# Optimization experiments

Hardware: AMD Instinct MI355X
Metric: run time of the kernel (lower is better)

Reference implementation:

```python
import jax, jax.numpy as jnp
import numpy as np

DIM = 512
DIM_HEAD = 64
HEADS = 8
DIM_INNER = DIM_HEAD * HEADS
EPS = float(jnp.finfo(jnp.float32).eps)  # torch nn.RMSNorm default eps


def setup_inputs() -> dict:
    key = jax.random.key(0)
    k1, k2, k3, k4 = jax.random.split(key, 4)
    tokens = jax.random.normal(k1, (2, 4096, DIM), dtype=jnp.float32)
    norm_weight = jnp.ones((DIM,), dtype=jnp.float32)
    s = 1.0 / np.sqrt(DIM)
    w_qkv = jax.random.normal(k2, (DIM, 3 * DIM_INNER), dtype=jnp.float32) * s
    w_out = jax.random.normal(k3, (DIM_INNER, DIM), dtype=jnp.float32) * (1.0 / np.sqrt(DIM_INNER))
    return {"tokens": tokens, "norm_weight": norm_weight, "w_qkv": w_qkv, "w_out": w_out}


def reference(tokens, norm_weight, w_qkv, w_out):
    b, n, d = tokens.shape
    scale = DIM_HEAD ** -0.5
    # RMSNorm
    ms = jnp.mean(jnp.square(tokens), axis=-1, keepdims=True)
    x = tokens * jax.lax.rsqrt(ms + EPS) * norm_weight
    # QKV projection, split heads: b n (qkv h d) -> qkv b h n d
    qkv = x @ w_qkv                                   # [b, n, 3*h*dh]
    qkv = qkv.reshape(b, n, 3, HEADS, DIM_HEAD)
    q, k, v = jnp.moveaxis(qkv, 2, 0)                 # each [b, n, h, dh]
    q = jnp.swapaxes(q, 1, 2)                         # [b, h, n, dh]
    k = jnp.swapaxes(k, 1, 2)
    v = jnp.swapaxes(v, 1, 2)
    # naive attention (note: original applies no scale in forward, self.scale unused)
    sim = jnp.einsum('bhid,bhjd->bhij', q, k)
    attn = jax.nn.softmax(sim, axis=-1)
    out = jnp.einsum('bhij,bhjd->bhid', attn, v)
    out = jnp.swapaxes(out, 1, 2).reshape(b, n, DIM_INNER)
    return out @ w_out
```

## Files before the change

kernel.cpp:

```cpp
#include <hip/hip_runtime.h>
#include <stdint.h>
#include <stddef.h>

typedef _Float16 half_t;
typedef __attribute__((ext_vector_type(2))) __fp16 fp16v2;
typedef __attribute__((ext_vector_type(4))) _Float16 f16x4;
typedef __attribute__((ext_vector_type(8))) _Float16 f16x8;
typedef __attribute__((ext_vector_type(4))) float f32x4;

#define EPSF 1.1920928955078125e-07f
#define LOG2E 1.4426950408889634f

#define AS1 __attribute__((address_space(1)))
#define AS3 __attribute__((address_space(3)))

#define WS_XN   0u
#define WS_WQT  4194304u
#define WS_WOT  4980736u
#define WS_Q    5242880u
#define WS_K    9437184u
#define WS_VT   13631488u
#define WS_AO   17825792u
#define WS_NEED_BYTES 44040192u

__device__ __forceinline__ void gload16(const void* g, void* l) {
  __builtin_amdgcn_global_load_lds((const AS1 void*)g, (AS3 void*)l, 16, 0, 0);
}

__device__ __forceinline__ float fast_exp2(float x) {
#if __has_builtin(__builtin_amdgcn_exp2f)
  return __builtin_amdgcn_exp2f(x);
#else
  return exp2f(x);
#endif
}

__global__ __launch_bounds__(256) void k_rmsnorm(const float* __restrict__ t,
                                                 const float* __restrict__ w,
                                                 half_t* __restrict__ xn) {
  int row = blockIdx.x * 4 + (threadIdx.x >> 6);
  int ln = threadIdx.x & 63;
  const float* src = t + (size_t)row * 512 + ln * 8;
  float4 a = *(const float4*)src;
  float4 b = *(const float4*)(src + 4);
  float ss = a.x * a.x + a.y * a.y + a.z * a.z + a.w * a.w
           + b.x * b.x + b.y * b.y + b.z * b.z + b.w * b.w;
#pragma unroll
  for (int m = 32; m >= 1; m >>= 1) ss += __shfl_xor(ss, m);
  float r = rsqrtf(ss * (1.0f / 512.0f) + EPSF);
  const float* wp = w + ln * 8;
  float4 w0 = *(const float4*)wp;
  float4 w1 = *(const float4*)(wp + 4);
  f16x8 o;
  o[0] = (_Float16)(a.x * r * w0.x);
  o[1] = (_Float16)(a.y * r * w0.y);
  o[2] = (_Float16)(a.z * r * w0.z);
  o[3] = (_Float16)(a.w * r * w0.w);
  o[4] = (_Float16)(b.x * r * w1.x);
  o[5] = (_Float16)(b.y * r * w1.y);
  o[6] = (_Float16)(b.z * r * w1.z);
  o[7] = (_Float16)(b.w * r * w1.w);
  *(f16x8*)(xn + (size_t)row * 512 + ln * 8) = o;
}

__global__ void k_transpose_cast(const float* __restrict__ src, half_t* __restrict__ dst,
                                 int K, int N) {
  int idx = blockIdx.x * 256 + threadIdx.x;
  if (idx >= K * N) return;
  int n = idx / K, k = idx - n * K;
  dst[idx] = (_Float16)src[(size_t)k * N + n];
}

__device__ __forceinline__ void gemm_core(const half_t* __restrict__ A,
                                          const half_t* __restrict__ Bt,
                                          int m0, int n0, int Ksz,
                                          half_t* Al, half_t* Bl,
                                          f32x4 acc[4][4]) {
  int wv = threadIdx.x >> 6, ln = threadIdx.x & 63;
  int wm = (wv >> 1) << 6, wn = (wv & 1) << 6;
  for (int kt = 0; kt < Ksz; kt += 64) {
#pragma unroll
    for (int i = 0; i < 4; ++i) {
      int seg = wv * 4 + i;
      int r = seg * 8 + (ln >> 3);
      int cb = ((ln & 7) * 16) ^ ((r & 7) << 4);
      gload16((const char*)(A + (size_t)(m0 + r) * Ksz + kt) + cb, (char*)Al + seg * 1024);
      gload16((const char*)(Bt + (size_t)(n0 + r) * Ksz + kt) + cb, (char*)Bl + seg * 1024);
    }
    __syncthreads();
#pragma unroll
    for (int kc = 0; kc < 2; ++kc) {
      f16x8 af[4], bf[4];
#pragma unroll
      for (int mt = 0; mt < 4; ++mt) {
        int rr = wm + mt * 16 + (ln & 15);
        af[mt] = *(const f16x8*)((const char*)Al + rr * 128 +
                                 ((kc * 64 + (ln >> 4) * 16) ^ ((rr & 7) << 4)));
      }
#pragma unroll
      for (int nt = 0; nt < 4; ++nt) {
        int rr = wn + nt * 16 + (ln & 15);
        bf[nt] = *(const f16x8*)((const char*)Bl + rr * 128 +
                                 ((kc * 64 + (ln >> 4) * 16) ^ ((rr & 7) << 4)));
      }
#pragma unroll
      for (int mt = 0; mt < 4; ++mt)
#pragma unroll
        for (int nt = 0; nt < 4; ++nt)
          acc[mt][nt] = __builtin_amdgcn_mfma_f32_16x16x32_f16(af[mt], bf[nt], acc[mt][nt], 0, 0, 0);
    }
    __syncthreads();
  }
}

__global__ __launch_bounds__(256, 2) void k_gemm_qkv(const half_t* __restrict__ A,
                                                     const half_t* __restrict__ Bt,
                                                     half_t* __restrict__ q,
                                                     half_t* __restrict__ kk,
                                                     half_t* __restrict__ vt) {
  __shared__ __align__(16) half_t Al[128 * 64];
  __shared__ __align__(16) half_t Bl[128 * 64];
  f32x4 acc[4][4];
  f32x4 z = {0.f, 0.f, 0.f, 0.f};
#pragma unroll
  for (int i = 0; i < 4; ++i)
#pragma unroll
    for (int j = 0; j < 4; ++j) acc[i][j] = z;
  int m0 = blockIdx.x * 128, n0 = blockIdx.y * 128;
  gemm_core(A, Bt, m0, n0, 512, Al, Bl, acc);
  int wv = threadIdx.x >> 6, ln = threadIdx.x & 63;
  int wm = (wv >> 1) << 6, wn = (wv & 1) << 6;
#pragma unroll
  for (int mt = 0; mt < 4; ++mt) {
#pragma unroll
    for (int nt = 0; nt < 4; ++nt) {
      int gn = n0 + wn + nt * 16 + (ln & 15);
      int qkv_i = gn >> 9;
      int h = (gn >> 6) & 7;
      int d = gn & 63;
#pragma unroll
      for (int j = 0; j < 4; ++j) {
        int gm = m0 + wm + mt * 16 + (ln >> 4) * 4 + j;
        int head = ((gm >> 12) << 3) | h;
        int n = gm & 4095;
        float av = acc[mt][nt][j];
        if (qkv_i == 0)      q [((size_t)head * 4096 + n) * 64 + d] = (_Float16)(av * LOG2E);
        else if (qkv_i == 1) kk[((size_t)head * 4096 + n) * 64 + d] = (_Float16)av;
        else                 vt[((size_t)head * 64 + d) * 4096 + n] = (_Float16)av;
      }
    }
  }
}

__global__ __launch_bounds__(256, 2) void k_gemm_out(const half_t* __restrict__ A,
                                                     const half_t* __restrict__ Bt,
                                                     float* __restrict__ out) {
  __shared__ __align__(16) half_t Al[128 * 64];
  __shared__ __align__(16) half_t Bl[128 * 64];
  f32x4 acc[4][4];
  f32x4 z = {0.f, 0.f, 0.f, 0.f};
#pragma unroll
  for (int i = 0; i < 4; ++i)
#pragma unroll
    for (int j = 0; j < 4; ++j) acc[i][j] = z;
  int m0 = blockIdx.x * 128, n0 = blockIdx.y * 128;
  gemm_core(A, Bt, m0, n0, 512, Al, Bl, acc);
  int wv = threadIdx.x >> 6, ln = threadIdx.x & 63;
  int wm = (wv >> 1) << 6, wn = (wv & 1) << 6;
#pragma unroll
  for (int mt = 0; mt < 4; ++mt)
#pragma unroll
    for (int nt = 0; nt < 4; ++nt) {
      int gn = n0 + wn + nt * 16 + (ln & 15);
#pragma unroll
      for (int j = 0; j < 4; ++j) {
        int gm = m0 + wm + mt * 16 + (ln >> 4) * 4 + j;
        out[(size_t)gm * 512 + gn] = acc[mt][nt][j];
      }
    }
}

__global__ __launch_bounds__(256, 2) void k_attn(const half_t* __restrict__ q,
                                                 const half_t* __restrict__ kg,
                                                 const half_t* __restrict__ vt,
                                                 half_t* __restrict__ ao) {
  __shared__ __align__(16) char lds[32768];
  const int wv = threadIdx.x >> 6, ln = threadIdx.x & 63;
  const int bid = blockIdx.x;
  const int lin = (bid & 7) * 64 + (bid >> 3);
  const int head = lin >> 5;
  const int qt = lin & 31;
  const int q0 = qt * 128 + wv * 32;
  const char* qh = (const char*)(q  + (size_t)head * 4096 * 64);
  const char* kh = (const char*)(kg + (size_t)head * 4096 * 64);
  const char* vh = (const char*)(vt + (size_t)head * 64 * 4096);

  f16x8 qf[2][2];
#pragma unroll
  for (int mt = 0; mt < 2; ++mt)
#pragma unroll
    for (int kc = 0; kc < 2; ++kc) {
      int r = q0 + mt * 16 + (ln & 15);
      qf[mt][kc] = *(const f16x8*)(qh + (size_t)r * 128 + kc * 64 + (ln >> 4) * 16);
    }

  const char* ks[2]; const char* vs[2]; int lo[2];
#pragma unroll
  for (int i = 0; i < 2; ++i) {
    int seg = wv * 2 + i;
    int r = seg * 8 + (ln >> 3);
    int cb = ((ln & 7) * 16) ^ ((r & 7) << 4);
    ks[i] = kh + (size_t)r * 128 + cb;
    vs[i] = vh + (size_t)r * 8192 + cb;
    lo[i] = seg * 1024;
  }

  float mrun[2] = {-1e30f, -1e30f};
  float lsum[2] = {0.f, 0.f};
  f32x4 oacc[2][4];
  const f32x4 z = {0.f, 0.f, 0.f, 0.f};
#pragma unroll
  for (int mt = 0; mt < 2; ++mt)
#pragma unroll
    for (int dt = 0; dt < 4; ++dt) oacc[mt][dt] = z;

  {
    char* base = lds;
    gload16(ks[0], base + lo[0]); gload16(ks[1], base + lo[1]);
    gload16(vs[0], base + 8192 + lo[0]); gload16(vs[1], base + 8192 + lo[1]);
    ks[0] += 8192; ks[1] += 8192; vs[0] += 128; vs[1] += 128;
  }
  __syncthreads();

  int cur = 0;
#pragma unroll 1
  for (int t = 0; t < 64; ++t) {
    if (t < 63) {
      char* base = lds + (cur ^ 1) * 16384;
      gload16(ks[0], base + lo[0]); gload16(ks[1], base + lo[1]);
      gload16(vs[0], base + 8192 + lo[0]); gload16(vs[1], base + 8192 + lo[1]);
      ks[0] += 8192; ks[1] += 8192; vs[0] += 128; vs[1] += 128;
    }
    const char* Kb = lds + cur * 16384;
    const char* Vb = Kb + 8192;

    f32x4 s[2][4];
#pragma unroll
    for (int mt = 0; mt < 2; ++mt)
#pragma unroll
      for (int kt = 0; kt < 4; ++kt) s[mt][kt] = z;
    __builtin_amdgcn_s_setprio(1);
#pragma unroll
    for (int kc = 0; kc < 2; ++kc) {
      f16x8 kf[4];
#pragma unroll
      for (int kt = 0; kt < 4; ++kt) {
        int rr = kt * 16 + (ln & 15);
        kf[kt] = *(const f16x8*)(Kb + rr * 128 + ((kc * 64 + (ln >> 4) * 16) ^ ((rr & 7) << 4)));
      }
#pragma unroll
      for (int mt = 0; mt < 2; ++mt)
#pragma unroll
        for (int kt = 0; kt < 4; ++kt)
          s[mt][kt] = __builtin_amdgcn_mfma_f32_16x16x32_f16(kf[kt], qf[mt][kc], s[mt][kt], 0, 0, 0);
    }
    __builtin_amdgcn_s_setprio(0);

    f16x8 pf[2][2];
#pragma unroll
    for (int mt = 0; mt < 2; ++mt) {
      float a0 = fmaxf(fmaxf(s[mt][0][0], s[mt][0][1]), fmaxf(s[mt][0][2], s[mt][0][3]));
      float a1 = fmaxf(fmaxf(s[mt][1][0], s[mt][1][1]), fmaxf(s[mt][1][2], s[mt][1][3]));
      float a2 = fmaxf(fmaxf(s[mt][2][0], s[mt][2][1]), fmaxf(s[mt][2][2], s[mt][2][3]));
      float a3 = fmaxf(fmaxf(s[mt][3][0], s[mt][3][1]), fmaxf(s[mt][3][2], s[mt][3][3]));
      float tm = fmaxf(fmaxf(a0, a1), fmaxf(a2, a3));
      tm = fmaxf(tm, __shfl_xor(tm, 16));
      tm = fmaxf(tm, __shfl_xor(tm, 32));
      if (__any(tm > mrun[mt] + 11.0f)) {
        float mnew = fmaxf(mrun[mt], tm);
        float sc = fast_exp2(mrun[mt] - mnew);
        mrun[mt] = mnew;
        lsum[mt] *= sc;
#pragma unroll
        for (int dt = 0; dt < 4; ++dt) {
          oacc[mt][dt][0] *= sc; oacc[mt][dt][1] *= sc;
          oacc[mt][dt][2] *= sc; oacc[mt][dt][3] *= sc;
        }
      }
      float p[4][4];
#pragma unroll
      for (int kt = 0; kt < 4; ++kt)
#pragma unroll
        for (int r = 0; r < 4; ++r) p[kt][r] = fast_exp2(s[mt][kt][r] - mrun[mt]);
      float ps = 0.f;
#pragma unroll
      for (int kt = 0; kt < 4; ++kt)
        ps += (p[kt][0] + p[kt][1]) + (p[kt][2] + p[kt][3]);
      lsum[mt] += ps;
#pragma unroll
      for (int kc = 0; kc < 2; ++kc) {
        union { f16x8 v; fp16v2 h[4]; } u;
        u.h[0] = __builtin_amdgcn_cvt_pkrtz(p[2 * kc][0], p[2 * kc][1]);
        u.h[1] = __builtin_amdgcn_cvt_pkrtz(p[2 * kc][2], p[2 * kc][3]);
        u.h[2] = __builtin_amdgcn_cvt_pkrtz(p[2 * kc + 1][0], p[2 * kc + 1][1]);
        u.h[3] = __builtin_amdgcn_cvt_pkrtz(p[2 * kc + 1][2], p[2 * kc + 1][3]);
        pf[mt][kc] = u.v;
      }
    }

    __builtin_amdgcn_s_setprio(1);
#pragma unroll
    for (int kc = 0; kc < 2; ++kc)
#pragma unroll
      for (int dt = 0; dt < 4; ++dt) {
        int rr = dt * 16 + (ln & 15);
        int sw = (rr & 7) << 4;
        f16x4 vlo = *(const f16x4*)(Vb + rr * 128 + ((kc * 64 + (ln >> 4) * 8) ^ sw));
        f16x4 vhi = *(const f16x4*)(Vb + rr * 128 + ((kc * 64 + 32 + (ln >> 4) * 8) ^ sw));
        f16x8 vf = __builtin_shufflevector(vlo, vhi, 0, 1, 2, 3, 4, 5, 6, 7);
#pragma unroll
        for (int mt = 0; mt < 2; ++mt)
          oacc[mt][dt] = __builtin_amdgcn_mfma_f32_16x16x32_f16(vf, pf[mt][kc], oacc[mt][dt], 0, 0, 0);
      }
    __builtin_amdgcn_s_setprio(0);

    __syncthreads();
    cur ^= 1;
  }

  const int b = head >> 3, h = head & 7;
#pragma unroll
  for (int mt = 0; mt < 2; ++mt) {
    float l = lsum[mt];
    l += __shfl_xor(l, 16);
    l += __shfl_xor(l, 32);
    float inv = 1.0f / l;
    int n = q0 + mt * 16 + (ln & 15);
    half_t* dst = ao + ((size_t)(b * 4096 + n)) * 512 + h * 64 + (ln >> 4) * 4;
#pragma unroll
    for (int dt = 0; dt < 4; ++dt) {
      f16x4 o4;
      o4[0] = (_Float16)(oacc[mt][dt][0] * inv);
      o4[1] = (_Float16)(oacc[mt][dt][1] * inv);
      o4[2] = (_Float16)(oacc[mt][dt][2] * inv);
      o4[3] = (_Float16)(oacc[mt][dt][3] * inv);
      *(f16x4*)(dst + dt * 16) = o4;
    }
  }
}

extern "C" void kernel_launch(void* const* d_in, const int* in_sizes, int n_in,
                              void* d_out, int out_size, void* d_ws, size_t ws_size,
                              hipStream_t stream) {
  if (ws_size < WS_NEED_BYTES) return;
  const float* tokens = (const float*)d_in[0];
  const float* nw     = (const float*)d_in[1];
  const float* wqkv   = (const float*)d_in[2];
  const float* wout   = (const float*)d_in[3];
  float* out = (float*)d_out;
  half_t* ws = (half_t*)d_ws;
  half_t* xn  = ws + WS_XN;
  half_t* wqt = ws + WS_WQT;
  half_t* wot = ws + WS_WOT;
  half_t* qb  = ws + WS_Q;
  half_t* kb  = ws + WS_K;
  half_t* vtb = ws + WS_VT;
  half_t* aob = ws + WS_AO;

  k_rmsnorm<<<2048, 256, 0, stream>>>(tokens, nw, xn);
  k_transpose_cast<<<(1536 * 512 + 255) / 256, 256, 0, stream>>>(wqkv, wqt, 512, 1536);
  k_transpose_cast<<<(512 * 512 + 255) / 256, 256, 0, stream>>>(wqkv ? wout : wout, wot, 512, 512);
  k_gemm_qkv<<<dim3(64, 12), 256, 0, stream>>>(xn, wqt, qb, kb, vtb);
  k_attn<<<512, 256, 0, stream>>>(qb, kb, vtb, aob);
  k_gemm_out<<<dim3(64, 4), 256, 0, stream>>>(aob, wot, out);
}
```

Measured before the change: 152.9 us.

## Load K tiles straight into registers and compute row sums with MFMA

The attention kernel stops staging K through LDS. Each wave now reads its K fragments directly from global memory into double-buffered registers, one tile ahead, so LDS holds only V and shrinks to 16 KB. The softmax row-sum is accumulated with an extra MFMA against a ones vector, which removes the scalar sums and cross-lane shuffles at the end. V fragment reads are also moved ahead of the softmax math. The cost is that all four waves fetch the same K tile from global/L2, plus higher register pressure and extra tail prefetches past the last tile.

```diff
diff --git a/kernel.cpp b/kernel.cpp
--- a/kernel.cpp
+++ b/kernel.cpp
@@ -184,7 +184,7 @@
                                                  const half_t* __restrict__ kg,
                                                  const half_t* __restrict__ vt,
                                                  half_t* __restrict__ ao) {
-  __shared__ __align__(16) char lds[32768];
+  __shared__ __align__(16) char lds[16384];
   const int wv = threadIdx.x >> 6, ln = threadIdx.x & 63;
   const int bid = blockIdx.x;
   const int lin = (bid & 7) * 64 + (bid >> 3);
@@ -204,137 +204,148 @@
       qf[mt][kc] = *(const f16x8*)(qh + (size_t)r * 128 + kc * 64 + (ln >> 4) * 16);
     }
 
-  const char* ks[2]; const char* vs[2]; int lo[2];
+  const char* kbl = kh + (size_t)(ln & 15) * 128 + (ln >> 4) * 16;
+
+  const char* vs[2]; int lo[2];
 #pragma unroll
   for (int i = 0; i < 2; ++i) {
     int seg = wv * 2 + i;
     int r = seg * 8 + (ln >> 3);
     int cb = ((ln & 7) * 16) ^ ((r & 7) << 4);
-    ks[i] = kh + (size_t)r * 128 + cb;
     vs[i] = vh + (size_t)r * 8192 + cb;
     lo[i] = seg * 1024;
   }
 
   float mrun[2] = {-1e30f, -1e30f};
-  float lsum[2] = {0.f, 0.f};
   f32x4 oacc[2][4];
+  f32x4 lacc[2];
   const f32x4 z = {0.f, 0.f, 0.f, 0.f};
 #pragma unroll
-  for (int mt = 0; mt < 2; ++mt)
+  for (int mt = 0; mt < 2; ++mt) {
+    lacc[mt] = z;
 #pragma unroll
     for (int dt = 0; dt < 4; ++dt) oacc[mt][dt] = z;
-
-  {
-    char* base = lds;
-    gload16(ks[0], base + lo[0]); gload16(ks[1], base + lo[1]);
-    gload16(vs[0], base + 8192 + lo[0]); gload16(vs[1], base + 8192 + lo[1]);
-    ks[0] += 8192; ks[1] += 8192; vs[0] += 128; vs[1] += 128;
-  }
+  }
+  f16x8 ones;
+#pragma unroll
+  for (int e = 0; e < 8; ++e) ones[e] = (_Float16)1.0f;
+
+  f16x8 kA[4][2], kB[4][2];
+
+#define KLOAD(DST, TT) do {                                        \
+    const char* _kb = kbl + (size_t)(TT) * 8192;                   \
+    DST[0][0] = *(const f16x8*)(_kb);                              \
+    DST[0][1] = *(const f16x8*)(_kb + 64);                         \
+    DST[1][0] = *(const f16x8*)(_kb + 2048);                       \
+    DST[1][1] = *(const f16x8*)(_kb + 2112);                       \
+    DST[2][0] = *(const f16x8*)(_kb + 4096);                       \
+    DST[2][1] = *(const f16x8*)(_kb + 4160);                       \
+    DST[3][0] = *(const f16x8*)(_kb + 6144);                       \
+    DST[3][1] = *(const f16x8*)(_kb + 6208);                       \
+  } while (0)
+
+  KLOAD(kA, 0);
+  gload16(vs[0], lds + lo[0]); gload16(vs[1], lds + lo[1]);
+  vs[0] += 128; vs[1] += 128;
   __syncthreads();
 
-  int cur = 0;
+#define TILE_PHASE(KCUR, KNXT, T) {                                            \
+       \
+    KLOAD(KNXT, (T) + 1);                                                      \
+    { char* _base = lds + (((T) + 1) & 1) * 8192;                              \
+      gload16(vs[0], _base + lo[0]); gload16(vs[1], _base + lo[1]);            \
+      vs[0] += 128; vs[1] += 128; }                                            \
+    const char* Vb = lds + ((T) & 1) * 8192;                                   \
+                                                            \
+    f32x4 s[2][4];                                                             \
+    _Pragma("unroll") for (int mt = 0; mt < 2; ++mt)                           \
+      _Pragma("unroll") for (int kt = 0; kt < 4; ++kt) s[mt][kt] = z;          \
+    __builtin_amdgcn_s_setprio(1);                                             \
+    _Pragma("unroll") for (int kc = 0; kc < 2; ++kc)                           \
+      _Pragma("unroll") for (int mt = 0; mt < 2; ++mt)                         \
+        _Pragma("unroll") for (int kt = 0; kt < 4; ++kt)                       \
+          s[mt][kt] = __builtin_amdgcn_mfma_f32_16x16x32_f16(                  \
+              KCUR[kt][kc], qf[mt][kc], s[mt][kt], 0, 0, 0);                   \
+    __builtin_amdgcn_s_setprio(0);                                             \
+                      \
+    f16x8 vf0[4], vf1[4];                                                      \
+    _Pragma("unroll") for (int dt = 0; dt < 4; ++dt) {                         \
+      int rr = dt * 16 + (ln & 15);                                            \
+      int sw = (rr & 7) << 4;                                                  \
+      f16x4 a_ = *(const f16x4*)(Vb + rr * 128 + (((ln >> 4) * 8) ^ sw));      \
+      f16x4 b_ = *(const f16x4*)(Vb + rr * 128 + ((32 + (ln >> 4) * 8) ^ sw)); \
+      vf0[dt] = __builtin_shufflevector(a_, b_, 0, 1, 2, 3, 4, 5, 6, 7);       \
+      f16x4 c_ = *(const f16x4*)(Vb + rr * 128 + ((64 + (ln >> 4) * 8) ^ sw)); \
+      f16x4 d_ = *(const f16x4*)(Vb + rr * 128 + ((96 + (ln >> 4) * 8) ^ sw)); \
+      vf1[dt] = __builtin_shufflevector(c_, d_, 0, 1, 2, 3, 4, 5, 6, 7);       \
+    }                                                                          \
+                      \
+    f16x8 pf[2][2];                                                            \
+    _Pragma("unroll") for (int mt = 0; mt < 2; ++mt) {                         \
+      float a0 = fmaxf(fmaxf(s[mt][0][0], s[mt][0][1]),                        \
+                       fmaxf(s[mt][0][2], s[mt][0][3]));                       \
+      float a1 = fmaxf(fmaxf(s[mt][1][0], s[mt][1][1]),                        \
+                       fmaxf(s[mt][1][2], s[mt][1][3]));                       \
+      float a2 = fmaxf(fmaxf(s[mt][2][0], s[mt][2][1]),                        \
+                       fmaxf(s[mt][2][2], s[mt][2][3]));                       \
+      float a3 = fmaxf(fmaxf(s[mt][3][0], s[mt][3][1]),                        \
+                       fmaxf(s[mt][3][2], s[mt][3][3]));                       \
+      float tm = fmaxf(fmaxf(a0, a1), fmaxf(a2, a3));                          \
+      tm = fmaxf(tm, __shfl_xor(tm, 16));                                      \
+      tm = fmaxf(tm, __shfl_xor(tm, 32));                                      \
+      if (__any(tm > mrun[mt] + 11.0f)) {                                      \
+        float mnew = fmaxf(mrun[mt], tm);                                      \
+        float sc = fast_exp2(mrun[mt] - mnew);                                 \
+        mrun[mt] = mnew;                                                       \
+        lacc[mt][0] *= sc;                                                     \
+        _Pragma("unroll") for (int dt = 0; dt < 4; ++dt) {                     \
+          oacc[mt][dt][0] *= sc; oacc[mt][dt][1] *= sc;                        \
+          oacc[mt][dt][2] *= sc; oacc[mt][dt][3] *= sc;                        \
+        }                                                                      \
+      }                                                                        \
+      float p[4][4];                                                           \
+      _Pragma("unroll") for (int kt = 0; kt < 4; ++kt)                         \
+        _Pragma("unroll") for (int r = 0; r < 4; ++r)                          \
+          p[kt][r] = fast_exp2(s[mt][kt][r] - mrun[mt]);                       \
+      _Pragma("unroll") for (int kc = 0; kc < 2; ++kc) {                       \
+        union { f16x8 v; fp16v2 h[4]; } u;                                     \
+        u.h[0] = __builtin_amdgcn_cvt_pkrtz(p[2 * kc][0], p[2 * kc][1]);       \
+        u.h[1] = __builtin_amdgcn_cvt_pkrtz(p[2 * kc][2], p[2 * kc][3]);       \
+        u.h[2] = __builtin_amdgcn_cvt_pkrtz(p[2 * kc + 1][0], p[2 * kc + 1][1]); \
+        u.h[3] = __builtin_amdgcn_cvt_pkrtz(p[2 * kc + 1][2], p[2 * kc + 1][3]); \
+        pf[mt][kc] = u.v;                                                      \
+      }                                                                        \
+    }                                                                          \
+     \
+    __builtin_amdgcn_s_setprio(1);                                             \
+    _Pragma("unroll") for (int dt = 0; dt < 4; ++dt)                           \
+      _Pragma("unroll") for (int mt = 0; mt < 2; ++mt)                         \
+        oacc[mt][dt] = __builtin_amdgcn_mfma_f32_16x16x32_f16(                 \
+            vf0[dt], pf[mt][0], oacc[mt][dt], 0, 0, 0);                        \
+    lacc[0] = __builtin_amdgcn_mfma_f32_16x16x32_f16(ones, pf[0][0], lacc[0], 0, 0, 0); \
+    lacc[1] = __builtin_amdgcn_mfma_f32_16x16x32_f16(ones, pf[1][0], lacc[1], 0, 0, 0); \
+    _Pragma("unroll") for (int dt = 0; dt < 4; ++dt)                           \
+      _Pragma("unroll") for (int mt = 0; mt < 2; ++mt)                         \
+        oacc[mt][dt] = __builtin_amdgcn_mfma_f32_16x16x32_f16(                 \
+            vf1[dt], pf[mt][1], oacc[mt][dt], 0, 0, 0);                        \
+    lacc[0] = __builtin_amdgcn_mfma_f32_16x16x32_f16(ones, pf[0][1], lacc[0], 0, 0, 0); \
+    lacc[1] = __builtin_amdgcn_mfma_f32_16x16x32_f16(ones, pf[1][1], lacc[1], 0, 0, 0); \
+    __builtin_amdgcn_s_setprio(0);                                             \
+    __syncthreads();                                                           \
+  }
+
 #pragma unroll 1
-  for (int t = 0; t < 64; ++t) {
-    if (t < 63) {
-      char* base = lds + (cur ^ 1) * 16384;
-      gload16(ks[0], base + lo[0]); gload16(ks[1], base + lo[1]);
-      gload16(vs[0], base + 8192 + lo[0]); gload16(vs[1], base + 8192 + lo[1]);
-      ks[0] += 8192; ks[1] += 8192; vs[0] += 128; vs[1] += 128;
-    }
-    const char* Kb = lds + cur * 16384;
-    const char* Vb = Kb + 8192;
-
-    f32x4 s[2][4];
-#pragma unroll
-    for (int mt = 0; mt < 2; ++mt)
-#pragma unroll
-      for (int kt = 0; kt < 4; ++kt) s[mt][kt] = z;
-    __builtin_amdgcn_s_setprio(1);
-#pragma unroll
-    for (int kc = 0; kc < 2; ++kc) {
-      f16x8 kf[4];
-#pragma unroll
-      for (int kt = 0; kt < 4; ++kt) {
-        int rr = kt * 16 + (ln & 15);
-        kf[kt] = *(const f16x8*)(Kb + rr * 128 + ((kc * 64 + (ln >> 4) * 16) ^ ((rr & 7) << 4)));
-      }
-#pragma unroll
-      for (int mt = 0; mt < 2; ++mt)
-#pragma unroll
-        for (int kt = 0; kt < 4; ++kt)
-          s[mt][kt] = __builtin_amdgcn_mfma_f32_16x16x32_f16(kf[kt], qf[mt][kc], s[mt][kt], 0, 0, 0);
-    }
-    __builtin_amdgcn_s_setprio(0);
-
-    f16x8 pf[2][2];
-#pragma unroll
-    for (int mt = 0; mt < 2; ++mt) {
-      float a0 = fmaxf(fmaxf(s[mt][0][0], s[mt][0][1]), fmaxf(s[mt][0][2], s[mt][0][3]));
-      float a1 = fmaxf(fmaxf(s[mt][1][0], s[mt][1][1]), fmaxf(s[mt][1][2], s[mt][1][3]));
-      float a2 = fmaxf(fmaxf(s[mt][2][0], s[mt][2][1]), fmaxf(s[mt][2][2], s[mt][2][3]));
-      float a3 = fmaxf(fmaxf(s[mt][3][0], s[mt][3][1]), fmaxf(s[mt][3][2], s[mt][3][3]));
-      float tm = fmaxf(fmaxf(a0, a1), fmaxf(a2, a3));
-      tm = fmaxf(tm, __shfl_xor(tm, 16));
-      tm = fmaxf(tm, __shfl_xor(tm, 32));
-      if (__any(tm > mrun[mt] + 11.0f)) {
-        float mnew = fmaxf(mrun[mt], tm);
-        float sc = fast_exp2(mrun[mt] - mnew);
-        mrun[mt] = mnew;
-        lsum[mt] *= sc;
-#pragma unroll
-        for (int dt = 0; dt < 4; ++dt) {
-          oacc[mt][dt][0] *= sc; oacc[mt][dt][1] *= sc;
-          oacc[mt][dt][2] *= sc; oacc[mt][dt][3] *= sc;
-        }
-      }
-      float p[4][4];
-#pragma unroll
-      for (int kt = 0; kt < 4; ++kt)
-#pragma unroll
-        for (int r = 0; r < 4; ++r) p[kt][r] = fast_exp2(s[mt][kt][r] - mrun[mt]);
-      float ps = 0.f;
-#pragma unroll
-      for (int kt = 0; kt < 4; ++kt)
-        ps += (p[kt][0] + p[kt][1]) + (p[kt][2] + p[kt][3]);
-      lsum[mt] += ps;
-#pragma unroll
-      for (int kc = 0; kc < 2; ++kc) {
-        union { f16x8 v; fp16v2 h[4]; } u;
-        u.h[0] = __builtin_amdgcn_cvt_pkrtz(p[2 * kc][0], p[2 * kc][1]);
-        u.h[1] = __builtin_amdgcn_cvt_pkrtz(p[2 * kc][2], p[2 * kc][3]);
-        u.h[2] = __builtin_amdgcn_cvt_pkrtz(p[2 * kc + 1][0], p[2 * kc + 1][1]);
-        u.h[3] = __builtin_amdgcn_cvt_pkrtz(p[2 * kc + 1][2], p[2 * kc + 1][3]);
-        pf[mt][kc] = u.v;
-      }
-    }
-
-    __builtin_amdgcn_s_setprio(1);
-#pragma unroll
-    for (int kc = 0; kc < 2; ++kc)
-#pragma unroll
-      for (int dt = 0; dt < 4; ++dt) {
-        int rr = dt * 16 + (ln & 15);
-        int sw = (rr & 7) << 4;
-        f16x4 vlo = *(const f16x4*)(Vb + rr * 128 + ((kc * 64 + (ln >> 4) * 8) ^ sw));
-        f16x4 vhi = *(const f16x4*)(Vb + rr * 128 + ((kc * 64 + 32 + (ln >> 4) * 8) ^ sw));
-        f16x8 vf = __builtin_shufflevector(vlo, vhi, 0, 1, 2, 3, 4, 5, 6, 7);
-#pragma unroll
-        for (int mt = 0; mt < 2; ++mt)
-          oacc[mt][dt] = __builtin_amdgcn_mfma_f32_16x16x32_f16(vf, pf[mt][kc], oacc[mt][dt], 0, 0, 0);
-      }
-    __builtin_amdgcn_s_setprio(0);
-
-    __syncthreads();
-    cur ^= 1;
-  }
+  for (int i = 0; i < 32; ++i) {
+    TILE_PHASE(kA, kB, 2 * i);
+    TILE_PHASE(kB, kA, 2 * i + 1);
+  }
+#undef TILE_PHASE
+#undef KLOAD
 
   const int b = head >> 3, h = head & 7;
 #pragma unroll
   for (int mt = 0; mt < 2; ++mt) {
-    float l = lsum[mt];
-    l += __shfl_xor(l, 16);
-    l += __shfl_xor(l, 32);
-    float inv = 1.0f / l;
+    float inv = 1.0f / lacc[mt][0];
     int n = q0 + mt * 16 + (ln & 15);
     half_t* dst = ao + ((size_t)(b * 4096 + n)) * 512 + h * 64 + (ln >> 4) * 4;
 #pragma unroll
@@ -369,7 +380,7 @@
 
   k_rmsnorm<<<2048, 256, 0, stream>>>(tokens, nw, xn);
   k_transpose_cast<<<(1536 * 512 + 255) / 256, 256, 0, stream>>>(wqkv, wqt, 512, 1536);
-  k_transpose_cast<<<(512 * 512 + 255) / 256, 256, 0, stream>>>(wqkv ? wout : wout, wot, 512, 512);
+  k_transpose_cast<<<(512 * 512 + 255) / 256, 256, 0, stream>>>(wout, wot, 512, 512);
   k_gemm_qkv<<<dim3(64, 12), 256, 0, stream>>>(xn, wqt, qb, kb, vtb);
   k_attn<<<512, 256, 0, stream>>>(qb, kb, vtb, aob);
   k_gemm_out<<<dim3(64, 4), 256, 0, stream>>>(aob, wot, out);
```

Result: slower. 177.7 us (+16.2%).

## Split attention KV range in two with combine pass and MFMA row sums

Applied to the files above, without the earlier changes.

Attention is split into two halves of the key/value sequence, which doubles the grid to 1024 blocks. Each half writes unnormalized partial outputs plus running max and sum, and a new combine kernel merges them. The softmax row sums are now computed with an MFMA against a ones vector instead of scalar adds. V fragment loads are hoisted ahead of the softmax, and occupancy is raised to 4 blocks. The out-projection GEMM reads the head-major combined output directly through a new addressing mode. The cost is an extra kernel launch, extra memory traffic for the partials, and reuse of workspace regions.

```diff
diff --git a/kernel.cpp b/kernel.cpp
--- a/kernel.cpp
+++ b/kernel.cpp
@@ -20,7 +20,7 @@
 #define WS_Q    5242880u
 #define WS_K    9437184u
 #define WS_VT   13631488u
-#define WS_AO   17825792u
+#define WS_O1   17825792u
 #define WS_NEED_BYTES 44040192u
 
 __device__ __forceinline__ void gload16(const void* g, void* l) {
@@ -71,6 +71,7 @@
   dst[idx] = (_Float16)src[(size_t)k * N + n];
 }
 
+template <int AMODE>
 __device__ __forceinline__ void gemm_core(const half_t* __restrict__ A,
                                           const half_t* __restrict__ Bt,
                                           int m0, int n0, int Ksz,
@@ -84,7 +85,15 @@
       int seg = wv * 4 + i;
       int r = seg * 8 + (ln >> 3);
       int cb = ((ln & 7) * 16) ^ ((r & 7) << 4);
-      gload16((const char*)(A + (size_t)(m0 + r) * Ksz + kt) + cb, (char*)Al + seg * 1024);
+      const char* asrc;
+      if constexpr (AMODE == 0) {
+        asrc = (const char*)(A + (size_t)(m0 + r) * Ksz + kt) + cb;
+      } else {
+        int gm = m0 + r;
+        asrc = (const char*)(A + (((size_t)((gm >> 12) * 8 + (kt >> 6)) * 4096 +
+                                   (gm & 4095)) * 64)) + cb;
+      }
+      gload16(asrc, (char*)Al + seg * 1024);
       gload16((const char*)(Bt + (size_t)(n0 + r) * Ksz + kt) + cb, (char*)Bl + seg * 1024);
     }
     __syncthreads();
@@ -127,7 +136,7 @@
 #pragma unroll
     for (int j = 0; j < 4; ++j) acc[i][j] = z;
   int m0 = blockIdx.x * 128, n0 = blockIdx.y * 128;
-  gemm_core(A, Bt, m0, n0, 512, Al, Bl, acc);
+  gemm_core<0>(A, Bt, m0, n0, 512, Al, Bl, acc);
   int wv = threadIdx.x >> 6, ln = threadIdx.x & 63;
   int wm = (wv >> 1) << 6, wn = (wv & 1) << 6;
 #pragma unroll
@@ -164,7 +173,7 @@
 #pragma unroll
     for (int j = 0; j < 4; ++j) acc[i][j] = z;
   int m0 = blockIdx.x * 128, n0 = blockIdx.y * 128;
-  gemm_core(A, Bt, m0, n0, 512, Al, Bl, acc);
+  gemm_core<1>(A, Bt, m0, n0, 512, Al, Bl, acc);
   int wv = threadIdx.x >> 6, ln = threadIdx.x & 63;
   int wm = (wv >> 1) << 6, wn = (wv & 1) << 6;
 #pragma unroll
@@ -180,20 +189,23 @@
     }
 }
 
-__global__ __launch_bounds__(256, 2) void k_attn(const half_t* __restrict__ q,
+__global__ __launch_bounds__(256, 4) void k_attn(const half_t* __restrict__ q,
                                                  const half_t* __restrict__ kg,
                                                  const half_t* __restrict__ vt,
-                                                 half_t* __restrict__ ao) {
+                                                 half_t* __restrict__ o0,
+                                                 half_t* __restrict__ o1,
+                                                 float* __restrict__ ml) {
   __shared__ __align__(16) char lds[32768];
   const int wv = threadIdx.x >> 6, ln = threadIdx.x & 63;
   const int bid = blockIdx.x;
-  const int lin = (bid & 7) * 64 + (bid >> 3);
-  const int head = lin >> 5;
-  const int qt = lin & 31;
+  const int lin = (bid & 7) * 128 + (bid >> 3);
+  const int head = lin >> 6;
+  const int qt = (lin >> 1) & 31;
+  const int kvh = lin & 1;
   const int q0 = qt * 128 + wv * 32;
   const char* qh = (const char*)(q  + (size_t)head * 4096 * 64);
-  const char* kh = (const char*)(kg + (size_t)head * 4096 * 64);
-  const char* vh = (const char*)(vt + (size_t)head * 64 * 4096);
+  const char* kh = (const char*)(kg + (size_t)head * 4096 * 64) + (size_t)kvh * 2048 * 128;
+  const char* vh = (const char*)(vt + (size_t)head * 64 * 4096) + (size_t)kvh * 2048 * 2;
 
   f16x8 qf[2][2];
 #pragma unroll
@@ -216,13 +228,18 @@
   }
 
   float mrun[2] = {-1e30f, -1e30f};
-  float lsum[2] = {0.f, 0.f};
   f32x4 oacc[2][4];
+  f32x4 lacc[2];
   const f32x4 z = {0.f, 0.f, 0.f, 0.f};
 #pragma unroll
-  for (int mt = 0; mt < 2; ++mt)
+  for (int mt = 0; mt < 2; ++mt) {
+    lacc[mt] = z;
 #pragma unroll
     for (int dt = 0; dt < 4; ++dt) oacc[mt][dt] = z;
+  }
+  f16x8 ones;
+#pragma unroll
+  for (int e = 0; e < 8; ++e) ones[e] = (_Float16)1.0f;
 
   {
     char* base = lds;
@@ -234,8 +251,8 @@
 
   int cur = 0;
 #pragma unroll 1
-  for (int t = 0; t < 64; ++t) {
-    if (t < 63) {
+  for (int t = 0; t < 32; ++t) {
+    if (t < 31) {
       char* base = lds + (cur ^ 1) * 16384;
       gload16(ks[0], base + lo[0]); gload16(ks[1], base + lo[1]);
       gload16(vs[0], base + 8192 + lo[0]); gload16(vs[1], base + 8192 + lo[1]);
@@ -265,6 +282,19 @@
           s[mt][kt] = __builtin_amdgcn_mfma_f32_16x16x32_f16(kf[kt], qf[mt][kc], s[mt][kt], 0, 0, 0);
     }
     __builtin_amdgcn_s_setprio(0);
+
+    f16x8 vf0[4], vf1[4];
+#pragma unroll
+    for (int dt = 0; dt < 4; ++dt) {
+      int rr = dt * 16 + (ln & 15);
+      int sw = (rr & 7) << 4;
+      f16x4 a_ = *(const f16x4*)(Vb + rr * 128 + (((ln >> 4) * 8) ^ sw));
+      f16x4 b_ = *(const f16x4*)(Vb + rr * 128 + ((32 + (ln >> 4) * 8) ^ sw));
+      vf0[dt] = __builtin_shufflevector(a_, b_, 0, 1, 2, 3, 4, 5, 6, 7);
+      f16x4 c_ = *(const f16x4*)(Vb + rr * 128 + ((64 + (ln >> 4) * 8) ^ sw));
+      f16x4 d_ = *(const f16x4*)(Vb + rr * 128 + ((96 + (ln >> 4) * 8) ^ sw));
+      vf1[dt] = __builtin_shufflevector(c_, d_, 0, 1, 2, 3, 4, 5, 6, 7);
+    }
 
     f16x8 pf[2][2];
 #pragma unroll
@@ -280,7 +310,7 @@
         float mnew = fmaxf(mrun[mt], tm);
         float sc = fast_exp2(mrun[mt] - mnew);
         mrun[mt] = mnew;
-        lsum[mt] *= sc;
+        lacc[mt][0] *= sc;
 #pragma unroll
         for (int dt = 0; dt < 4; ++dt) {
           oacc[mt][dt][0] *= sc; oacc[mt][dt][1] *= sc;
@@ -292,11 +322,6 @@
       for (int kt = 0; kt < 4; ++kt)
 #pragma unroll
         for (int r = 0; r < 4; ++r) p[kt][r] = fast_exp2(s[mt][kt][r] - mrun[mt]);
-      float ps = 0.f;
-#pragma unroll
-      for (int kt = 0; kt < 4; ++kt)
-        ps += (p[kt][0] + p[kt][1]) + (p[kt][2] + p[kt][3]);
-      lsum[mt] += ps;
 #pragma unroll
       for (int kc = 0; kc < 2; ++kc) {
         union { f16x8 v; fp16v2 h[4]; } u;
@@ -310,43 +335,74 @@
 
     __builtin_amdgcn_s_setprio(1);
 #pragma unroll
-    for (int kc = 0; kc < 2; ++kc)
-#pragma unroll
-      for (int dt = 0; dt < 4; ++dt) {
-        int rr = dt * 16 + (ln & 15);
-        int sw = (rr & 7) << 4;
-        f16x4 vlo = *(const f16x4*)(Vb + rr * 128 + ((kc * 64 + (ln >> 4) * 8) ^ sw));
-        f16x4 vhi = *(const f16x4*)(Vb + rr * 128 + ((kc * 64 + 32 + (ln >> 4) * 8) ^ sw));
-        f16x8 vf = __builtin_shufflevector(vlo, vhi, 0, 1, 2, 3, 4, 5, 6, 7);
-#pragma unroll
-        for (int mt = 0; mt < 2; ++mt)
-          oacc[mt][dt] = __builtin_amdgcn_mfma_f32_16x16x32_f16(vf, pf[mt][kc], oacc[mt][dt], 0, 0, 0);
-      }
+    for (int dt = 0; dt < 4; ++dt)
+#pragma unroll
+      for (int mt = 0; mt < 2; ++mt)
+        oacc[mt][dt] = __builtin_amdgcn_mfma_f32_16x16x32_f16(vf0[dt], pf[mt][0], oacc[mt][dt], 0, 0, 0);
+    lacc[0] = __builtin_amdgcn_mfma_f32_16x16x32_f16(ones, pf[0][0], lacc[0], 0, 0, 0);
+    lacc[1] = __builtin_amdgcn_mfma_f32_16x16x32_f16(ones, pf[1][0], lacc[1], 0, 0, 0);
+#pragma unroll
+    for (int dt = 0; dt < 4; ++dt)
+#pragma unroll
+      for (int mt = 0; mt < 2; ++mt)
+        oacc[mt][dt] = __builtin_amdgcn_mfma_f32_16x16x32_f16(vf1[dt], pf[mt][1], oacc[mt][dt], 0, 0, 0);
+    lacc[0] = __builtin_amdgcn_mfma_f32_16x16x32_f16(ones, pf[0][1], lacc[0], 0, 0, 0);
+    lacc[1] = __builtin_amdgcn_mfma_f32_16x16x32_f16(ones, pf[1][1], lacc[1], 0, 0, 0);
     __builtin_amdgcn_s_setprio(0);
 
     __syncthreads();
     cur ^= 1;
   }
 
-  const int b = head >> 3, h = head & 7;
+  half_t* op = kvh ? o1 : o0;
+  float* Mh = ml + (size_t)kvh * 2 * 65536;
 #pragma unroll
   for (int mt = 0; mt < 2; ++mt) {
-    float l = lsum[mt];
-    l += __shfl_xor(l, 16);
-    l += __shfl_xor(l, 32);
-    float inv = 1.0f / l;
     int n = q0 + mt * 16 + (ln & 15);
-    half_t* dst = ao + ((size_t)(b * 4096 + n)) * 512 + h * 64 + (ln >> 4) * 4;
+    size_t row = (size_t)head * 4096 + n;
+    half_t* dst = op + row * 64 + (ln >> 4) * 4;
 #pragma unroll
     for (int dt = 0; dt < 4; ++dt) {
       f16x4 o4;
-      o4[0] = (_Float16)(oacc[mt][dt][0] * inv);
-      o4[1] = (_Float16)(oacc[mt][dt][1] * inv);
-      o4[2] = (_Float16)(oacc[mt][dt][2] * inv);
-      o4[3] = (_Float16)(oacc[mt][dt][3] * inv);
+      o4[0] = (_Float16)oacc[mt][dt][0];
+      o4[1] = (_Float16)oacc[mt][dt][1];
+      o4[2] = (_Float16)oacc[mt][dt][2];
+      o4[3] = (_Float16)oacc[mt][dt][3];
       *(f16x4*)(dst + dt * 16) = o4;
     }
-  }
+    if ((ln >> 4) == 0) {
+      Mh[row] = mrun[mt];
+      Mh[65536 + row] = lacc[mt][0];
+    }
+  }
+}
+
+__global__ __launch_bounds__(256) void k_combine(half_t* __restrict__ o0,
+                                                 const half_t* __restrict__ o1,
+                                                 const float* __restrict__ ml) {
+  int tid = blockIdx.x * 256 + threadIdx.x;
+  int row = tid >> 2;
+  int c = (tid & 3) * 16;
+  float m0 = ml[row],          l0 = ml[65536 + row];
+  float m1 = ml[131072 + row], l1 = ml[196608 + row];
+  float M = fmaxf(m0, m1);
+  float s0 = fast_exp2(m0 - M), s1 = fast_exp2(m1 - M);
+  float inv = 1.0f / (l0 * s0 + l1 * s1);
+  float a0 = s0 * inv, a1 = s1 * inv;
+  half_t* p0 = o0 + (size_t)row * 64 + c;
+  const half_t* p1 = o1 + (size_t)row * 64 + c;
+  f16x8 x0 = *(const f16x8*)p0;
+  f16x8 x1 = *(const f16x8*)p1;
+  f16x8 y0 = *(const f16x8*)(p0 + 8);
+  f16x8 y1 = *(const f16x8*)(p1 + 8);
+  f16x8 r0, r1;
+#pragma unroll
+  for (int e = 0; e < 8; ++e) {
+    r0[e] = (_Float16)((float)x0[e] * a0 + (float)x1[e] * a1);
+    r1[e] = (_Float16)((float)y0[e] * a0 + (float)y1[e] * a1);
+  }
+  *(f16x8*)p0 = r0;
+  *(f16x8*)(p0 + 8) = r1;
 }
 
 extern "C" void kernel_launch(void* const* d_in, const int* in_sizes, int n_in,
@@ -365,12 +421,14 @@
   half_t* qb  = ws + WS_Q;
   half_t* kb  = ws + WS_K;
   half_t* vtb = ws + WS_VT;
-  half_t* aob = ws + WS_AO;
+  half_t* o1b = ws + WS_O1;
+  float*  mlb = (float*)(ws + WS_WQT);
 
   k_rmsnorm<<<2048, 256, 0, stream>>>(tokens, nw, xn);
   k_transpose_cast<<<(1536 * 512 + 255) / 256, 256, 0, stream>>>(wqkv, wqt, 512, 1536);
-  k_transpose_cast<<<(512 * 512 + 255) / 256, 256, 0, stream>>>(wqkv ? wout : wout, wot, 512, 512);
+  k_transpose_cast<<<(512 * 512 + 255) / 256, 256, 0, stream>>>(wout, wot, 512, 512);
   k_gemm_qkv<<<dim3(64, 12), 256, 0, stream>>>(xn, wqt, qb, kb, vtb);
-  k_attn<<<512, 256, 0, stream>>>(qb, kb, vtb, aob);
-  k_gemm_out<<<dim3(64, 4), 256, 0, stream>>>(aob, wot, out);
-}
+  k_attn<<<1024, 256, 0, stream>>>(qb, kb, vtb, xn , o1b, mlb);
+  k_combine<<<1024, 256, 0, stream>>>(xn , o1b, mlb);
+  k_gemm_out<<<dim3(64, 4), 256, 0, stream>>>(xn , wot, out);
+}
```

Result: slower. 197.5 us (+29.2%).

## Permute V columns for 16-byte LDS reads and compute row sums via MFMA

Applied to the files above, without the earlier changes.

The QKV GEMM now writes the transposed V with a permuted column order inside each 32-key chunk. This lets the attention kernel load each V fragment with one 16-byte LDS read instead of two 8-byte reads plus a shuffle, and all V fragments are loaded before the softmax work. The softmax row sum is now accumulated by extra MFMAs against a vector of ones instead of scalar adds and cross-lane shuffles. This moves VALU work onto the matrix unit at the cost of four extra MFMAs per tile and more registers held live for V.

```diff
diff --git a/kernel.cpp b/kernel.cpp
--- a/kernel.cpp
+++ b/kernel.cpp
@@ -146,7 +146,10 @@
         float av = acc[mt][nt][j];
         if (qkv_i == 0)      q [((size_t)head * 4096 + n) * 64 + d] = (_Float16)(av * LOG2E);
         else if (qkv_i == 1) kk[((size_t)head * 4096 + n) * 64 + d] = (_Float16)av;
-        else                 vt[((size_t)head * 64 + d) * 4096 + n] = (_Float16)av;
+        else {
+          int pcol = (n & ~31) | (((n >> 2) & 3) << 3) | (((n >> 4) & 1) << 2) | (n & 3);
+          vt[((size_t)head * 64 + d) * 4096 + pcol] = (_Float16)av;
+        }
       }
     }
   }
@@ -216,13 +219,18 @@
   }
 
   float mrun[2] = {-1e30f, -1e30f};
-  float lsum[2] = {0.f, 0.f};
   f32x4 oacc[2][4];
+  f32x4 lacc[2];
   const f32x4 z = {0.f, 0.f, 0.f, 0.f};
 #pragma unroll
-  for (int mt = 0; mt < 2; ++mt)
+  for (int mt = 0; mt < 2; ++mt) {
+    lacc[mt] = z;
 #pragma unroll
     for (int dt = 0; dt < 4; ++dt) oacc[mt][dt] = z;
+  }
+  f16x8 ones;
+#pragma unroll
+  for (int e = 0; e < 8; ++e) ones[e] = (_Float16)1.0f;
 
   {
     char* base = lds;
@@ -265,6 +273,15 @@
           s[mt][kt] = __builtin_amdgcn_mfma_f32_16x16x32_f16(kf[kt], qf[mt][kc], s[mt][kt], 0, 0, 0);
     }
     __builtin_amdgcn_s_setprio(0);
+
+    f16x8 vf[2][4];
+#pragma unroll
+    for (int dt = 0; dt < 4; ++dt) {
+      int rr = dt * 16 + (ln & 15);
+      int sw = (rr & 7) << 4;
+      vf[0][dt] = *(const f16x8*)(Vb + rr * 128 + (((ln >> 4) * 16) ^ sw));
+      vf[1][dt] = *(const f16x8*)(Vb + rr * 128 + ((64 + (ln >> 4) * 16) ^ sw));
+    }
 
     f16x8 pf[2][2];
 #pragma unroll
@@ -280,7 +297,7 @@
         float mnew = fmaxf(mrun[mt], tm);
         float sc = fast_exp2(mrun[mt] - mnew);
         mrun[mt] = mnew;
-        lsum[mt] *= sc;
+        lacc[mt][0] *= sc;
 #pragma unroll
         for (int dt = 0; dt < 4; ++dt) {
           oacc[mt][dt][0] *= sc; oacc[mt][dt][1] *= sc;
@@ -292,11 +309,6 @@
       for (int kt = 0; kt < 4; ++kt)
 #pragma unroll
         for (int r = 0; r < 4; ++r) p[kt][r] = fast_exp2(s[mt][kt][r] - mrun[mt]);
-      float ps = 0.f;
-#pragma unroll
-      for (int kt = 0; kt < 4; ++kt)
-        ps += (p[kt][0] + p[kt][1]) + (p[kt][2] + p[kt][3]);
-      lsum[mt] += ps;
 #pragma unroll
       for (int kc = 0; kc < 2; ++kc) {
         union { f16x8 v; fp16v2 h[4]; } u;
@@ -310,18 +322,19 @@
 
     __builtin_amdgcn_s_setprio(1);
 #pragma unroll
-    for (int kc = 0; kc < 2; ++kc)
-#pragma unroll
-      for (int dt = 0; dt < 4; ++dt) {
-        int rr = dt * 16 + (ln & 15);
-        int sw = (rr & 7) << 4;
-        f16x4 vlo = *(const f16x4*)(Vb + rr * 128 + ((kc * 64 + (ln >> 4) * 8) ^ sw));
-        f16x4 vhi = *(const f16x4*)(Vb + rr * 128 + ((kc * 64 + 32 + (ln >> 4) * 8) ^ sw));
-        f16x8 vf = __builtin_shufflevector(vlo, vhi, 0, 1, 2, 3, 4, 5, 6, 7);
-#pragma unroll
-        for (int mt = 0; mt < 2; ++mt)
-          oacc[mt][dt] = __builtin_amdgcn_mfma_f32_16x16x32_f16(vf, pf[mt][kc], oacc[mt][dt], 0, 0, 0);
-      }
+    for (int dt = 0; dt < 4; ++dt)
+#pragma unroll
+      for (int mt = 0; mt < 2; ++mt)
+        oacc[mt][dt] = __builtin_amdgcn_mfma_f32_16x16x32_f16(vf[0][dt], pf[mt][0], oacc[mt][dt], 0, 0, 0);
+    lacc[0] = __builtin_amdgcn_mfma_f32_16x16x32_f16(ones, pf[0][0], lacc[0], 0, 0, 0);
+    lacc[1] = __builtin_amdgcn_mfma_f32_16x16x32_f16(ones, pf[1][0], lacc[1], 0, 0, 0);
+#pragma unroll
+    for (int dt = 0; dt < 4; ++dt)
+#pragma unroll
+      for (int mt = 0; mt < 2; ++mt)
+        oacc[mt][dt] = __builtin_amdgcn_mfma_f32_16x16x32_f16(vf[1][dt], pf[mt][1], oacc[mt][dt], 0, 0, 0);
+    lacc[0] = __builtin_amdgcn_mfma_f32_16x16x32_f16(ones, pf[0][1], lacc[0], 0, 0, 0);
+    lacc[1] = __builtin_amdgcn_mfma_f32_16x16x32_f16(ones, pf[1][1], lacc[1], 0, 0, 0);
     __builtin_amdgcn_s_setprio(0);
 
     __syncthreads();
@@ -331,10 +344,7 @@
   const int b = head >> 3, h = head & 7;
 #pragma unroll
   for (int mt = 0; mt < 2; ++mt) {
-    float l = lsum[mt];
-    l += __shfl_xor(l, 16);
-    l += __shfl_xor(l, 32);
-    float inv = 1.0f / l;
+    float inv = 1.0f / lacc[mt][0];
     int n = q0 + mt * 16 + (ln & 15);
     half_t* dst = ao + ((size_t)(b * 4096 + n)) * 512 + h * 64 + (ln >> 4) * 4;
 #pragma unroll
@@ -369,7 +379,7 @@
 
   k_rmsnorm<<<2048, 256, 0, stream>>>(tokens, nw, xn);
   k_transpose_cast<<<(1536 * 512 + 255) / 256, 256, 0, stream>>>(wqkv, wqt, 512, 1536);
-  k_transpose_cast<<<(512 * 512 + 255) / 256, 256, 0, stream>>>(wqkv ? wout : wout, wot, 512, 512);
+  k_transpose_cast<<<(512 * 512 + 255) / 256, 256, 0, stream>>>(wout, wot, 512, 512);
   k_gemm_qkv<<<dim3(64, 12), 256, 0, stream>>>(xn, wqt, qb, kb, vtb);
   k_attn<<<512, 256, 0, stream>>>(qb, kb, vtb, aob);
   k_gemm_out<<<dim3(64, 4), 256, 0, stream>>>(aob, wot, out);
```

Result: faster. 142.9 us (-6.5%).
